# Kernel optimization log

Measured on AMD Instinct MI355X. Metric: run time of the kernel, lower is better.

## Reference

```python
import jax, jax.numpy as jnp
import numpy as np

B, C, L, D = 8, 16, 256, 512
DIM_HEAD = 64
SCALE = DIM_HEAD ** -0.5


def setup_inputs() -> dict:
    key = jax.random.key(0)
    ks = jax.random.split(key, 9)
    s = 0.05  # small init scale to keep activations sane
    return {
        "x": jax.random.normal(ks[0], (B, C, L, D), jnp.float32),
        "w_qkv": jax.random.normal(ks[1], (D, 3 * D), jnp.float32) * s,
        "pos_emb": jax.random.normal(ks[2], (1, C, L, L), jnp.float32),
        "w1": jax.random.normal(ks[3], (L, L), jnp.float32) * s,
        "b1": jnp.zeros((L,), jnp.float32),
        "w2": jax.random.normal(ks[4], (L, 1), jnp.float32) * s,
        "b2": jnp.zeros((1,), jnp.float32),
        "w_out": jax.random.normal(ks[5], (D, D), jnp.float32) * s,
        "b_out": jnp.zeros((D,), jnp.float32),
    }


def reference(x, w_qkv, pos_emb, w1, b1, w2, b2, w_out, b_out):
    # squared index distance |j - i|^2, shape [1,1,L,L]
    idx = jnp.arange(L, dtype=x.dtype)
    dist = ((idx[None, :] - idx[:, None]) ** 2)[None, None]

    qkv = jnp.einsum('bcld,de->bcle', x, w_qkv)  # [B,C,L,3D]
    q, k, v = jnp.split(qkv, 3, axis=-1)

    dots = jnp.einsum('bcld,bcmd->bclm', q, k) * SCALE  # [B,C,L,L]
    attn = jax.nn.softmax(dots, axis=-1)

    # per-row adaptive variance via small MLP over the score row
    attn_weight = attn + pos_emb                         # [B,C,L,L]
    h = jax.nn.relu(attn_weight @ w1 + b1)               # [B,C,L,L]
    w = h @ w2 + b2                                      # [B,C,L,1]

    # Gaussian distance decay, then second softmax
    weight = jnp.exp(-dist / (2.0 * w * w + 1e-6))       # [B,C,L,L]
    attn2 = jax.nn.softmax(attn * weight, axis=-1)

    out = jnp.einsum('bclm,bcmd->bcld', attn2, v)        # [B,C,L,D]
    return out @ w_out + b_out
```

## Files before the change

### kernel.cpp

```cpp
#include <hip/hip_runtime.h>
#include <hip/hip_bf16.h>

typedef unsigned short u16;
typedef unsigned int u32;

typedef short bf16x8 __attribute__((ext_vector_type(8)));
typedef float f32x4 __attribute__((ext_vector_type(4)));

__device__ __forceinline__ u16 f2bf(float f) {
    union { float f; u32 u; } v; v.f = f;
    u32 u = v.u;
    return (u16)((u + 0x7fffu + ((u >> 16) & 1u)) >> 16);
}
__device__ __forceinline__ float bf2f(u16 b) {
    union { u32 u; float f; } v; v.u = ((u32)b) << 16;
    return v.f;
}

__device__ __forceinline__ void gload16(const u16* g, u16* lds_uniform_base, int lane) {
#if __has_builtin(__builtin_amdgcn_global_load_lds)
    __builtin_amdgcn_global_load_lds((const __attribute__((address_space(1))) void*)g,
                                     (__attribute__((address_space(3))) void*)lds_uniform_base,
                                     16, 0, 0);
#else
    *(int4*)(lds_uniform_base + lane * 8) = *(const int4*)g;
#endif
}

#define MFMA_BF16 __builtin_amdgcn_mfma_f32_16x16x32_bf16

__global__ __launch_bounds__(256) void qkv_k(
    const u16* __restrict__ A, const u16* __restrict__ B, u16* __restrict__ C)
{
    __shared__ u16 As[2][4096];
    __shared__ u16 Bs[2][4096];
    const int tid  = threadIdx.x;
    const int lane = tid & 63;
    const int wave = tid >> 6;
    const int wm = (wave >> 1) * 64, wn = (wave & 1) * 64;
    const int row0 = blockIdx.x * 128;
    const int col0 = blockIdx.y * 128;
    const u16* Bb = B + (size_t)blockIdx.z * 262144;
    u16* Cb = C + (size_t)blockIdx.z * 16777216;
    const int l15 = lane & 15, l4 = lane >> 4;
    const int slotp = l4 ^ (lane & 3) ^ ((lane >> 2) & 3);

    f32x4 acc[4][4] = {};

    auto stage = [&](int buf, int k0) {
        #pragma unroll
        for (int i = 0; i < 2; ++i) {
            int idx = tid + i * 256;
            int r = idx >> 2, c = idx & 3;
            int s = c ^ (r & 3) ^ ((r >> 2) & 3);
            gload16(A + (size_t)(row0 + r) * 512 + k0 + s * 8, &As[buf][(idx & ~63) * 8], lane);
        }
        #pragma unroll
        for (int i = 0; i < 2; ++i) {
            int idx = tid + i * 256;
            int r = idx >> 2, c = idx & 3;
            int s = c ^ (r & 3) ^ ((r >> 2) & 3);
            gload16(Bb + (size_t)(col0 + r) * 512 + k0 + s * 8, &Bs[buf][(idx & ~63) * 8], lane);
        }
    };

    stage(0, 0);
    __syncthreads();
    for (int t = 0; t < 16; ++t) {
        int cur = t & 1;
        if (t < 15) stage(cur ^ 1, (t + 1) * 32);
        bf16x8 a[4], b[4];
        #pragma unroll
        for (int m = 0; m < 4; ++m)
            a[m] = *(const bf16x8*)&As[cur][(wm + m * 16 + l15) * 32 + slotp * 8];
        #pragma unroll
        for (int n = 0; n < 4; ++n)
            b[n] = *(const bf16x8*)&Bs[cur][(wn + n * 16 + l15) * 32 + slotp * 8];
        #pragma unroll
        for (int m = 0; m < 4; ++m)
            #pragma unroll
            for (int n = 0; n < 4; ++n)
                acc[m][n] = MFMA_BF16(a[m], b[n], acc[m][n], 0, 0, 0);
        __syncthreads();
    }

    #pragma unroll
    for (int m = 0; m < 4; ++m)
        #pragma unroll
        for (int n = 0; n < 4; ++n)
            #pragma unroll
            for (int r = 0; r < 4; ++r)
                Cb[(size_t)(row0 + wm + m * 16 + l4 * 4 + r) * 512 + col0 + wn + n * 16 + l15]
                    = f2bf(acc[m][n][r]);
}

__device__ __forceinline__ void stageB256(const u16* __restrict__ src, int ld, int k0,
                                          u16* buf, int tid, int lane) {
    #pragma unroll
    for (int i = 0; i < 4; ++i) {
        int idx = tid + i * 256;
        int r = idx >> 2, c = idx & 3;
        int s = c ^ (r & 3) ^ ((r >> 2) & 3);
        gload16(src + (size_t)r * ld + k0 + s * 8, &buf[(idx & ~63) * 8], lane);
    }
}
__device__ __forceinline__ void stageA64(const u16* __restrict__ src, int k0,
                                         u16* buf, int tid, int lane) {
    int r = tid >> 2, c = tid & 3;
    int s = c ^ (r & 3) ^ ((r >> 2) & 3);
    gload16(src + (size_t)r * 512 + k0 + s * 8, &buf[(tid & ~63) * 8], lane);
}

__device__ __forceinline__ int wswz(int row, int chunk) {
    return (chunk & 24) | ((chunk ^ row) & 7);
}
__device__ __forceinline__ bf16x8 rdW(const u16* W, int row, int chunk) {
    return *(const bf16x8*)&W[row * 256 + wswz(row, chunk) * 8];
}
__device__ __forceinline__ void wrW(u16* W, int row, int col, u16 v) {
    W[row * 256 + wswz(row, col >> 3) * 8 + (col & 7)] = v;
}

template<bool INIT>
__device__ __forceinline__ void gemm_from_W(
    f32x4 (&dst)[4][4], const u16* __restrict__ Bsrc, int ldb, int K,
    const u16* __restrict__ W, u16 (&Bs)[2][8192],
    int tid, int lane, int wn, int l15, int l4, int slotp)
{
    if (INIT)
        #pragma unroll
        for (int m = 0; m < 4; ++m)
            #pragma unroll
            for (int n = 0; n < 4; ++n) dst[m][n] = f32x4{0.f, 0.f, 0.f, 0.f};
    stageB256(Bsrc, ldb, 0, Bs[0], tid, lane);
    __syncthreads();
    const int nt = K >> 5;
    for (int t = 0; t < nt; ++t) {
        int cur = t & 1;
        if (t + 1 < nt) stageB256(Bsrc, ldb, (t + 1) * 32, Bs[cur ^ 1], tid, lane);
        bf16x8 a[4], b[4];
        #pragma unroll
        for (int m = 0; m < 4; ++m)
            a[m] = rdW(W, m * 16 + l15, t * 4 + l4);
        #pragma unroll
        for (int n = 0; n < 4; ++n)
            b[n] = *(const bf16x8*)&Bs[cur][(wn + n * 16 + l15) * 32 + slotp * 8];
        #pragma unroll
        for (int m = 0; m < 4; ++m)
            #pragma unroll
            for (int n = 0; n < 4; ++n)
                dst[m][n] = MFMA_BF16(a[m], b[n], dst[m][n], 0, 0, 0);
        __syncthreads();
    }
}

__device__ __forceinline__ void row_softmax(
    f32x4 (&val)[4][4], float (&red)[64][4], int wid, int l15, int l4)
{
    float rm[4][4];
    #pragma unroll
    for (int m = 0; m < 4; ++m)
        #pragma unroll
        for (int rr = 0; rr < 4; ++rr) {
            float x = fmaxf(fmaxf(val[m][0][rr], val[m][1][rr]),
                            fmaxf(val[m][2][rr], val[m][3][rr]));
            #pragma unroll
            for (int o = 1; o < 16; o <<= 1) x = fmaxf(x, __shfl_xor(x, o, 64));
            rm[m][rr] = x;
        }
    if (l15 == 0)
        #pragma unroll
        for (int m = 0; m < 4; ++m)
            #pragma unroll
            for (int rr = 0; rr < 4; ++rr)
                red[m * 16 + l4 * 4 + rr][wid] = rm[m][rr];
    __syncthreads();
    #pragma unroll
    for (int m = 0; m < 4; ++m)
        #pragma unroll
        for (int rr = 0; rr < 4; ++rr) {
            float4 rv = *(const float4*)&red[m * 16 + l4 * 4 + rr][0];
            rm[m][rr] = fmaxf(fmaxf(rv.x, rv.y), fmaxf(rv.z, rv.w));
        }
    __syncthreads();
    float rs[4][4];
    #pragma unroll
    for (int m = 0; m < 4; ++m)
        #pragma unroll
        for (int rr = 0; rr < 4; ++rr) {
            float s = 0.f;
            #pragma unroll
            for (int n = 0; n < 4; ++n) {
                float e = __expf(val[m][n][rr] - rm[m][rr]);
                val[m][n][rr] = e;
                s += e;
            }
            #pragma unroll
            for (int o = 1; o < 16; o <<= 1) s += __shfl_xor(s, o, 64);
            rs[m][rr] = s;
        }
    if (l15 == 0)
        #pragma unroll
        for (int m = 0; m < 4; ++m)
            #pragma unroll
            for (int rr = 0; rr < 4; ++rr)
                red[m * 16 + l4 * 4 + rr][wid] = rs[m][rr];
    __syncthreads();
    #pragma unroll
    for (int m = 0; m < 4; ++m)
        #pragma unroll
        for (int rr = 0; rr < 4; ++rr) {
            float4 rv = *(const float4*)&red[m * 16 + l4 * 4 + rr][0];
            float inv = 1.f / (rv.x + rv.y + rv.z + rv.w);
            #pragma unroll
            for (int n = 0; n < 4; ++n) val[m][n][rr] *= inv;
        }
    __syncthreads();
}

__global__ __launch_bounds__(256, 2) void fused_k(
    const u16* __restrict__ qb, const u16* __restrict__ kb, const u16* __restrict__ vT,
    const u16* __restrict__ w1T, const u16* __restrict__ woT,
    const float* __restrict__ pos, const float* __restrict__ b1v,
    const float* __restrict__ w2v, const float* __restrict__ b2v,
    const float* __restrict__ bov, float* __restrict__ out)
{
    __shared__ u16 As[2][2048];
    __shared__ u16 Bs[2][8192];
    __shared__ u16 W[64 * 256];
    __shared__ float red[64][4];
    __shared__ float wr[64];

    const int tid  = threadIdx.x;
    const int lane = tid & 63;
    const int wid  = tid >> 6;
    const int wn   = wid * 64;
    const int l15 = lane & 15, l4 = lane >> 4;
    const int slotp = l4 ^ (lane & 3) ^ ((lane >> 2) & 3);

    int hw = blockIdx.x + (blockIdx.y << 2);
    int wg = ((hw & 7) << 6) | (hw >> 3);
    const int row0 = (wg & 3) * 64;
    const int z    = wg >> 2;

    const u16* q = qb + (size_t)z * 131072 + (size_t)row0 * 512;
    const u16* k = kb + (size_t)z * 131072;
    const u16* v = vT + (size_t)z * 131072;
    const float* posb = pos + (size_t)(z & 15) * 65536 + (size_t)row0 * 256;
    const float b2s = b2v[0];

    f32x4 sa[4][4] = {};
    f32x4 acc[4][4];

    stageA64(q, 0, As[0], tid, lane);
    stageB256(k, 512, 0, Bs[0], tid, lane);
    __syncthreads();
    for (int t = 0; t < 16; ++t) {
        int cur = t & 1;
        if (t < 15) {
            stageA64(q, (t + 1) * 32, As[cur ^ 1], tid, lane);
            stageB256(k, 512, (t + 1) * 32, Bs[cur ^ 1], tid, lane);
        }
        bf16x8 a[4], b[4];
        #pragma unroll
        for (int m = 0; m < 4; ++m)
            a[m] = *(const bf16x8*)&As[cur][(m * 16 + l15) * 32 + slotp * 8];
        #pragma unroll
        for (int n = 0; n < 4; ++n)
            b[n] = *(const bf16x8*)&Bs[cur][(wn + n * 16 + l15) * 32 + slotp * 8];
        #pragma unroll
        for (int m = 0; m < 4; ++m)
            #pragma unroll
            for (int n = 0; n < 4; ++n)
                sa[m][n] = MFMA_BF16(a[m], b[n], sa[m][n], 0, 0, 0);
        __syncthreads();
    }

    #pragma unroll
    for (int m = 0; m < 4; ++m)
        #pragma unroll
        for (int n = 0; n < 4; ++n) sa[m][n] *= 0.125f;
    row_softmax(sa, red, wid, l15, l4);
    #pragma unroll
    for (int m = 0; m < 4; ++m)
        #pragma unroll
        for (int rr = 0; rr < 4; ++rr) {
            int row = m * 16 + l4 * 4 + rr;
            #pragma unroll
            for (int n = 0; n < 4; ++n) {
                int col = wn + n * 16 + l15;
                wrW(W, row, col, f2bf(sa[m][n][rr] + posb[row * 256 + col]));
            }
        }

    float b1c[4], w2c[4];
    #pragma unroll
    for (int n = 0; n < 4; ++n) {
        int col = wn + n * 16 + l15;
        b1c[n] = b1v[col];
        w2c[n] = w2v[col];
    }
    gemm_from_W<true>(acc, w1T, 256, 256, W, Bs, tid, lane, wn, l15, l4, slotp);
    {
        float part[4][4];
        #pragma unroll
        for (int m = 0; m < 4; ++m)
            #pragma unroll
            for (int rr = 0; rr < 4; ++rr) {
                float p = 0.f;
                #pragma unroll
                for (int n = 0; n < 4; ++n)
                    p += fmaxf(acc[m][n][rr] + b1c[n], 0.f) * w2c[n];
                #pragma unroll
                for (int o = 1; o < 16; o <<= 1) p += __shfl_xor(p, o, 64);
                part[m][rr] = p;
            }
        if (l15 == 0)
            #pragma unroll
            for (int m = 0; m < 4; ++m)
                #pragma unroll
                for (int rr = 0; rr < 4; ++rr)
                    red[m * 16 + l4 * 4 + rr][wid] = part[m][rr];
        __syncthreads();
        if (wid == 0 && l15 == 0)
            #pragma unroll
            for (int m = 0; m < 4; ++m)
                #pragma unroll
                for (int rr = 0; rr < 4; ++rr) {
                    int row = m * 16 + l4 * 4 + rr;
                    float4 rv = *(const float4*)&red[row][0];
                    wr[row] = rv.x + rv.y + rv.z + rv.w + b2s;
                }
        __syncthreads();
    }

    #pragma unroll
    for (int m = 0; m < 4; ++m)
        #pragma unroll
        for (int rr = 0; rr < 4; ++rr) {
            int row = m * 16 + l4 * 4 + rr;
            float wv = wr[row];
            float idn = 1.f / (2.f * wv * wv + 1e-6f);
            int rg = row0 + row;
            #pragma unroll
            for (int n = 0; n < 4; ++n) {
                float d = (float)(wn + n * 16 + l15 - rg);
                sa[m][n][rr] *= __expf(-d * d * idn);
            }
        }
    row_softmax(sa, red, wid, l15, l4);
    #pragma unroll
    for (int m = 0; m < 4; ++m)
        #pragma unroll
        for (int rr = 0; rr < 4; ++rr) {
            int row = m * 16 + l4 * 4 + rr;
            #pragma unroll
            for (int n = 0; n < 4; ++n)
                wrW(W, row, wn + n * 16 + l15, f2bf(sa[m][n][rr]));
        }
    __syncthreads();

    gemm_from_W<true>(sa,  v,         256, 256, W, Bs, tid, lane, wn, l15, l4, slotp);
    gemm_from_W<true>(acc, v + 65536, 256, 256, W, Bs, tid, lane, wn, l15, l4, slotp);

    #pragma unroll
    for (int m = 0; m < 4; ++m)
        #pragma unroll
        for (int rr = 0; rr < 4; ++rr) {
            int row = m * 16 + l4 * 4 + rr;
            #pragma unroll
            for (int n = 0; n < 4; ++n)
                wrW(W, row, wn + n * 16 + l15, f2bf(sa[m][n][rr]));
        }
    f32x4 o0[4][4], o1[4][4];
    gemm_from_W<true>(o0, woT,                512, 256, W, Bs, tid, lane, wn, l15, l4, slotp);
    gemm_from_W<true>(o1, woT + 131072,       512, 256, W, Bs, tid, lane, wn, l15, l4, slotp);
    #pragma unroll
    for (int m = 0; m < 4; ++m)
        #pragma unroll
        for (int rr = 0; rr < 4; ++rr) {
            int row = m * 16 + l4 * 4 + rr;
            #pragma unroll
            for (int n = 0; n < 4; ++n)
                wrW(W, row, wn + n * 16 + l15, f2bf(acc[m][n][rr]));
        }
    gemm_from_W<false>(o0, woT + 256,          512, 256, W, Bs, tid, lane, wn, l15, l4, slotp);
    gemm_from_W<false>(o1, woT + 131072 + 256, 512, 256, W, Bs, tid, lane, wn, l15, l4, slotp);

    float bo0[4], bo1[4];
    #pragma unroll
    for (int n = 0; n < 4; ++n) {
        bo0[n] = bov[wn + n * 16 + l15];
        bo1[n] = bov[256 + wn + n * 16 + l15];
    }
    #pragma unroll
    for (int m = 0; m < 4; ++m)
        #pragma unroll
        for (int rr = 0; rr < 4; ++rr) {
            int row = row0 + m * 16 + l4 * 4 + rr;
            size_t ob = ((size_t)z * 256 + row) * 512;
            #pragma unroll
            for (int n = 0; n < 4; ++n) {
                out[ob + wn + n * 16 + l15]       = o0[m][n][rr] + bo0[n];
                out[ob + 256 + wn + n * 16 + l15] = o1[m][n][rr] + bo1[n];
            }
        }
}

__global__ __launch_bounds__(256) void trans_f2b_k(
    const float* __restrict__ in, u16* __restrict__ out, int R, int C)
{
    __shared__ u16 t[64][80];
    const int bx = blockIdx.x, by = blockIdx.y;
    const int tid = threadIdx.x;
    const int r = tid >> 2, c16 = (tid & 3) * 16;
    const float* ip = in + (size_t)(by * 64 + r) * C + bx * 64 + c16;
    #pragma unroll
    for (int j = 0; j < 4; ++j) {
        float4 vv = *(const float4*)(ip + j * 4);
        t[r][c16 + j * 4 + 0] = f2bf(vv.x);
        t[r][c16 + j * 4 + 1] = f2bf(vv.y);
        t[r][c16 + j * 4 + 2] = f2bf(vv.z);
        t[r][c16 + j * 4 + 3] = f2bf(vv.w);
    }
    __syncthreads();
    const int orow = tid >> 2, oc = (tid & 3) * 16;
    u16 o[16];
    #pragma unroll
    for (int j = 0; j < 16; ++j) o[j] = t[oc + j][orow];
    u16* op = out + (size_t)(bx * 64 + orow) * R + by * 64 + oc;
    *(int4*)op       = *(const int4*)&o[0];
    *(int4*)(op + 8) = *(const int4*)&o[8];
}

__global__ __launch_bounds__(256) void trans_b2b_k(
    const u16* __restrict__ in, u16* __restrict__ out,
    int ldin, int R, long sIn, long sOut)
{
    __shared__ u16 t[64][80];
    const int bx = blockIdx.x, by = blockIdx.y;
    const long zz = blockIdx.z;
    const u16* ip = in + zz * sIn;
    u16* op = out + zz * sOut;
    const int tid = threadIdx.x;
    const int r = tid >> 2, c16 = (tid & 3) * 16;
    const u16* src = ip + (size_t)(by * 64 + r) * ldin + bx * 64 + c16;
    *(int4*)&t[r][c16]     = *(const int4*)src;
    *(int4*)&t[r][c16 + 8] = *(const int4*)(src + 8);
    __syncthreads();
    const int orow = tid >> 2, oc = (tid & 3) * 16;
    u16 o[16];
    #pragma unroll
    for (int j = 0; j < 16; ++j) o[j] = t[oc + j][orow];
    u16* dst = op + (size_t)(bx * 64 + orow) * R + by * 64 + oc;
    *(int4*)dst       = *(const int4*)&o[0];
    *(int4*)(dst + 8) = *(const int4*)&o[8];
}

__global__ __launch_bounds__(256) void conv_b_k(
    const float* __restrict__ in, u16* __restrict__ out, int n8)
{
    int i = blockIdx.x * 256 + threadIdx.x;
    if (i >= n8) return;
    float4 a = ((const float4*)in)[i * 2], b = ((const float4*)in)[i * 2 + 1];
    u16 o[8] = { f2bf(a.x), f2bf(a.y), f2bf(a.z), f2bf(a.w),
                 f2bf(b.x), f2bf(b.y), f2bf(b.z), f2bf(b.w) };
    ((int4*)out)[i] = *(const int4*)o;
}

extern "C" void kernel_launch(void* const* d_in, const int* in_sizes, int n_in,
                              void* d_out, int out_size, void* d_ws, size_t ws_size,
                              hipStream_t stream) {
    const float* x     = (const float*)d_in[0];
    const float* w_qkv = (const float*)d_in[1];
    const float* pos   = (const float*)d_in[2];
    const float* w1    = (const float*)d_in[3];
    const float* b1    = (const float*)d_in[4];
    const float* w2    = (const float*)d_in[5];
    const float* b2    = (const float*)d_in[6];
    const float* w_out = (const float*)d_in[7];
    const float* b_out = (const float*)d_in[8];
    float* out = (float*)d_out;
    char* ws = (char*)d_ws;

    u16* xb    = (u16*)(ws);
    u16* vT    = (u16*)(ws);
    u16* qkvb  = (u16*)(ws + 33554432);
    u16* wqkvT = (u16*)(ws + 134217728);
    u16* w1T   = (u16*)(ws + 135790592);
    u16* woT   = (u16*)(ws + 135921664);
    if (ws_size < (size_t)136445952) return;

    u16* qb = qkvb;
    u16* kb = qkvb + 16777216;
    u16* vb = qkvb + 33554432;

    dim3 blk(256);

    conv_b_k<<<dim3(8192), blk, 0, stream>>>(x, xb, 2097152);
    trans_f2b_k<<<dim3(24, 8), blk, 0, stream>>>(w_qkv, wqkvT, 512, 1536);
    trans_f2b_k<<<dim3(4, 4), blk, 0, stream>>>(w1, w1T, 256, 256);
    trans_f2b_k<<<dim3(8, 8), blk, 0, stream>>>(w_out, woT, 512, 512);

    qkv_k<<<dim3(256, 4, 3), blk, 0, stream>>>(xb, wqkvT, qkvb);

    trans_b2b_k<<<dim3(8, 4, 128), blk, 0, stream>>>(vb, vT, 512, 256, 131072L, 131072L);

    fused_k<<<dim3(4, 128), blk, 0, stream>>>(
        qb, kb, vT, w1T, woT, pos, b1, w2, b2, b_out, out);
}
```

Baseline: 334.7 us.

## Replace LDS-staged operand tiles with direct global fragment loads in GEMMs

Removes the double-buffered LDS staging and global_load_lds paths for B operands (and Q/K and the QKV GEMM) so each wave reads MFMA fragments directly from global memory via L1/L2, dropping per-iteration barriers. The fused kernel now keeps two LDS attention/value tiles (Wa, Wb) and restructures the output projection into a loop over halves with fewer live accumulators. qkv_k gets a higher occupancy hint. This trades LDS traffic and syncs for uncoalesced-ish redundant global/cache loads across waves and less latency hiding.

```diff
diff --git a/kernel.cpp b/kernel.cpp
--- a/kernel.cpp
+++ b/kernel.cpp
@@ -17,23 +17,11 @@
     return v.f;
 }
 
-__device__ __forceinline__ void gload16(const u16* g, u16* lds_uniform_base, int lane) {
-#if __has_builtin(__builtin_amdgcn_global_load_lds)
-    __builtin_amdgcn_global_load_lds((const __attribute__((address_space(1))) void*)g,
-                                     (__attribute__((address_space(3))) void*)lds_uniform_base,
-                                     16, 0, 0);
-#else
-    *(int4*)(lds_uniform_base + lane * 8) = *(const int4*)g;
-#endif
-}
-
 #define MFMA_BF16 __builtin_amdgcn_mfma_f32_16x16x32_bf16
 
-__global__ __launch_bounds__(256) void qkv_k(
+__global__ __launch_bounds__(256, 3) void qkv_k(
     const u16* __restrict__ A, const u16* __restrict__ B, u16* __restrict__ C)
 {
-    __shared__ u16 As[2][4096];
-    __shared__ u16 Bs[2][4096];
     const int tid  = threadIdx.x;
     const int lane = tid & 63;
     const int wave = tid >> 6;
@@ -43,45 +31,26 @@
     const u16* Bb = B + (size_t)blockIdx.z * 262144;
     u16* Cb = C + (size_t)blockIdx.z * 16777216;
     const int l15 = lane & 15, l4 = lane >> 4;
-    const int slotp = l4 ^ (lane & 3) ^ ((lane >> 2) & 3);
+
+    const u16* Arow = A + (size_t)(row0 + wm + l15) * 512 + l4 * 8;
+    const u16* Brow = Bb + (size_t)(col0 + wn + l15) * 512 + l4 * 8;
 
     f32x4 acc[4][4] = {};
 
-    auto stage = [&](int buf, int k0) {
-        #pragma unroll
-        for (int i = 0; i < 2; ++i) {
-            int idx = tid + i * 256;
-            int r = idx >> 2, c = idx & 3;
-            int s = c ^ (r & 3) ^ ((r >> 2) & 3);
-            gload16(A + (size_t)(row0 + r) * 512 + k0 + s * 8, &As[buf][(idx & ~63) * 8], lane);
-        }
-        #pragma unroll
-        for (int i = 0; i < 2; ++i) {
-            int idx = tid + i * 256;
-            int r = idx >> 2, c = idx & 3;
-            int s = c ^ (r & 3) ^ ((r >> 2) & 3);
-            gload16(Bb + (size_t)(col0 + r) * 512 + k0 + s * 8, &Bs[buf][(idx & ~63) * 8], lane);
-        }
-    };
-
-    stage(0, 0);
-    __syncthreads();
+    #pragma unroll 4
     for (int t = 0; t < 16; ++t) {
-        int cur = t & 1;
-        if (t < 15) stage(cur ^ 1, (t + 1) * 32);
         bf16x8 a[4], b[4];
         #pragma unroll
         for (int m = 0; m < 4; ++m)
-            a[m] = *(const bf16x8*)&As[cur][(wm + m * 16 + l15) * 32 + slotp * 8];
+            a[m] = *(const bf16x8*)(Arow + (size_t)m * 16 * 512 + t * 32);
         #pragma unroll
         for (int n = 0; n < 4; ++n)
-            b[n] = *(const bf16x8*)&Bs[cur][(wn + n * 16 + l15) * 32 + slotp * 8];
+            b[n] = *(const bf16x8*)(Brow + (size_t)n * 16 * 512 + t * 32);
         #pragma unroll
         for (int m = 0; m < 4; ++m)
             #pragma unroll
             for (int n = 0; n < 4; ++n)
                 acc[m][n] = MFMA_BF16(a[m], b[n], acc[m][n], 0, 0, 0);
-        __syncthreads();
     }
 
     #pragma unroll
@@ -94,23 +63,6 @@
                     = f2bf(acc[m][n][r]);
 }
 
-__device__ __forceinline__ void stageB256(const u16* __restrict__ src, int ld, int k0,
-                                          u16* buf, int tid, int lane) {
-    #pragma unroll
-    for (int i = 0; i < 4; ++i) {
-        int idx = tid + i * 256;
-        int r = idx >> 2, c = idx & 3;
-        int s = c ^ (r & 3) ^ ((r >> 2) & 3);
-        gload16(src + (size_t)r * ld + k0 + s * 8, &buf[(idx & ~63) * 8], lane);
-    }
-}
-__device__ __forceinline__ void stageA64(const u16* __restrict__ src, int k0,
-                                         u16* buf, int tid, int lane) {
-    int r = tid >> 2, c = tid & 3;
-    int s = c ^ (r & 3) ^ ((r >> 2) & 3);
-    gload16(src + (size_t)r * 512 + k0 + s * 8, &buf[(tid & ~63) * 8], lane);
-}
-
 __device__ __forceinline__ int wswz(int row, int chunk) {
     return (chunk & 24) | ((chunk ^ row) & 7);
 }
@@ -122,35 +74,30 @@
 }
 
 template<bool INIT>
-__device__ __forceinline__ void gemm_from_W(
-    f32x4 (&dst)[4][4], const u16* __restrict__ Bsrc, int ldb, int K,
-    const u16* __restrict__ W, u16 (&Bs)[2][8192],
-    int tid, int lane, int wn, int l15, int l4, int slotp)
-{
-    if (INIT)
+__device__ __forceinline__ void gemm_WB(
+    f32x4 (&dst)[4][4], const u16* __restrict__ Wlds, const u16* __restrict__ Bg,
+    int ldb, int wn, int l15, int l4)
+{
+    if constexpr (INIT)
         #pragma unroll
         for (int m = 0; m < 4; ++m)
             #pragma unroll
             for (int n = 0; n < 4; ++n) dst[m][n] = f32x4{0.f, 0.f, 0.f, 0.f};
-    stageB256(Bsrc, ldb, 0, Bs[0], tid, lane);
-    __syncthreads();
-    const int nt = K >> 5;
-    for (int t = 0; t < nt; ++t) {
-        int cur = t & 1;
-        if (t + 1 < nt) stageB256(Bsrc, ldb, (t + 1) * 32, Bs[cur ^ 1], tid, lane);
+    const u16* Brow = Bg + (size_t)(wn + l15) * ldb + l4 * 8;
+    #pragma unroll 4
+    for (int t = 0; t < 8; ++t) {
         bf16x8 a[4], b[4];
         #pragma unroll
         for (int m = 0; m < 4; ++m)
-            a[m] = rdW(W, m * 16 + l15, t * 4 + l4);
+            a[m] = rdW(Wlds, m * 16 + l15, t * 4 + l4);
         #pragma unroll
         for (int n = 0; n < 4; ++n)
-            b[n] = *(const bf16x8*)&Bs[cur][(wn + n * 16 + l15) * 32 + slotp * 8];
+            b[n] = *(const bf16x8*)(Brow + (size_t)n * 16 * ldb + t * 32);
         #pragma unroll
         for (int m = 0; m < 4; ++m)
             #pragma unroll
             for (int n = 0; n < 4; ++n)
                 dst[m][n] = MFMA_BF16(a[m], b[n], dst[m][n], 0, 0, 0);
-        __syncthreads();
     }
 }
 
@@ -225,9 +172,8 @@
     const float* __restrict__ w2v, const float* __restrict__ b2v,
     const float* __restrict__ bov, float* __restrict__ out)
 {
-    __shared__ u16 As[2][2048];
-    __shared__ u16 Bs[2][8192];
-    __shared__ u16 W[64 * 256];
+    __shared__ u16 Wa[64 * 256];
+    __shared__ u16 Wb[64 * 256];
     __shared__ float red[64][4];
     __shared__ float wr[64];
 
@@ -236,7 +182,6 @@
     const int wid  = tid >> 6;
     const int wn   = wid * 64;
     const int l15 = lane & 15, l4 = lane >> 4;
-    const int slotp = l4 ^ (lane & 3) ^ ((lane >> 2) & 3);
 
     int hw = blockIdx.x + (blockIdx.y << 2);
     int wg = ((hw & 7) << 6) | (hw >> 3);
@@ -252,28 +197,24 @@
     f32x4 sa[4][4] = {};
     f32x4 acc[4][4];
 
-    stageA64(q, 0, As[0], tid, lane);
-    stageB256(k, 512, 0, Bs[0], tid, lane);
-    __syncthreads();
-    for (int t = 0; t < 16; ++t) {
-        int cur = t & 1;
-        if (t < 15) {
-            stageA64(q, (t + 1) * 32, As[cur ^ 1], tid, lane);
-            stageB256(k, 512, (t + 1) * 32, Bs[cur ^ 1], tid, lane);
-        }
-        bf16x8 a[4], b[4];
-        #pragma unroll
-        for (int m = 0; m < 4; ++m)
-            a[m] = *(const bf16x8*)&As[cur][(m * 16 + l15) * 32 + slotp * 8];
-        #pragma unroll
-        for (int n = 0; n < 4; ++n)
-            b[n] = *(const bf16x8*)&Bs[cur][(wn + n * 16 + l15) * 32 + slotp * 8];
-        #pragma unroll
-        for (int m = 0; m < 4; ++m)
-            #pragma unroll
-            for (int n = 0; n < 4; ++n)
-                sa[m][n] = MFMA_BF16(a[m], b[n], sa[m][n], 0, 0, 0);
-        __syncthreads();
+    {
+        const u16* qrow = q + (size_t)l15 * 512 + l4 * 8;
+        const u16* krow = k + (size_t)(wn + l15) * 512 + l4 * 8;
+        #pragma unroll 4
+        for (int t = 0; t < 16; ++t) {
+            bf16x8 a[4], b[4];
+            #pragma unroll
+            for (int m = 0; m < 4; ++m)
+                a[m] = *(const bf16x8*)(qrow + (size_t)m * 16 * 512 + t * 32);
+            #pragma unroll
+            for (int n = 0; n < 4; ++n)
+                b[n] = *(const bf16x8*)(krow + (size_t)n * 16 * 512 + t * 32);
+            #pragma unroll
+            for (int m = 0; m < 4; ++m)
+                #pragma unroll
+                for (int n = 0; n < 4; ++n)
+                    sa[m][n] = MFMA_BF16(a[m], b[n], sa[m][n], 0, 0, 0);
+        }
     }
 
     #pragma unroll
@@ -289,9 +230,10 @@
             #pragma unroll
             for (int n = 0; n < 4; ++n) {
                 int col = wn + n * 16 + l15;
-                wrW(W, row, col, f2bf(sa[m][n][rr] + posb[row * 256 + col]));
+                wrW(Wa, row, col, f2bf(sa[m][n][rr] + posb[row * 256 + col]));
             }
         }
+    __syncthreads();
 
     float b1c[4], w2c[4];
     #pragma unroll
@@ -300,7 +242,7 @@
         b1c[n] = b1v[col];
         w2c[n] = w2v[col];
     }
-    gemm_from_W<true>(acc, w1T, 256, 256, W, Bs, tid, lane, wn, l15, l4, slotp);
+    gemm_WB<true>(acc, Wa, w1T, 256, wn, l15, l4);
     {
         float part[4][4];
         #pragma unroll
@@ -356,13 +298,11 @@
             int row = m * 16 + l4 * 4 + rr;
             #pragma unroll
             for (int n = 0; n < 4; ++n)
-                wrW(W, row, wn + n * 16 + l15, f2bf(sa[m][n][rr]));
-        }
-    __syncthreads();
-
-    gemm_from_W<true>(sa,  v,         256, 256, W, Bs, tid, lane, wn, l15, l4, slotp);
-    gemm_from_W<true>(acc, v + 65536, 256, 256, W, Bs, tid, lane, wn, l15, l4, slotp);
-
+                wrW(Wa, row, wn + n * 16 + l15, f2bf(sa[m][n][rr]));
+        }
+    __syncthreads();
+
+    gemm_WB<true>(acc, Wa, v, 256, wn, l15, l4);
     #pragma unroll
     for (int m = 0; m < 4; ++m)
         #pragma unroll
@@ -370,11 +310,10 @@
             int row = m * 16 + l4 * 4 + rr;
             #pragma unroll
             for (int n = 0; n < 4; ++n)
-                wrW(W, row, wn + n * 16 + l15, f2bf(sa[m][n][rr]));
-        }
-    f32x4 o0[4][4], o1[4][4];
-    gemm_from_W<true>(o0, woT,                512, 256, W, Bs, tid, lane, wn, l15, l4, slotp);
-    gemm_from_W<true>(o1, woT + 131072,       512, 256, W, Bs, tid, lane, wn, l15, l4, slotp);
+                wrW(Wb, row, wn + n * 16 + l15, f2bf(acc[m][n][rr]));
+        }
+    gemm_WB<true>(acc, Wa, v + 65536, 256, wn, l15, l4);
+    __syncthreads();
     #pragma unroll
     for (int m = 0; m < 4; ++m)
         #pragma unroll
@@ -382,29 +321,28 @@
             int row = m * 16 + l4 * 4 + rr;
             #pragma unroll
             for (int n = 0; n < 4; ++n)
-                wrW(W, row, wn + n * 16 + l15, f2bf(acc[m][n][rr]));
-        }
-    gemm_from_W<false>(o0, woT + 256,          512, 256, W, Bs, tid, lane, wn, l15, l4, slotp);
-    gemm_from_W<false>(o1, woT + 131072 + 256, 512, 256, W, Bs, tid, lane, wn, l15, l4, slotp);
-
-    float bo0[4], bo1[4];
-    #pragma unroll
-    for (int n = 0; n < 4; ++n) {
-        bo0[n] = bov[wn + n * 16 + l15];
-        bo1[n] = bov[256 + wn + n * 16 + l15];
-    }
-    #pragma unroll
-    for (int m = 0; m < 4; ++m)
-        #pragma unroll
-        for (int rr = 0; rr < 4; ++rr) {
-            int row = row0 + m * 16 + l4 * 4 + rr;
-            size_t ob = ((size_t)z * 256 + row) * 512;
-            #pragma unroll
-            for (int n = 0; n < 4; ++n) {
-                out[ob + wn + n * 16 + l15]       = o0[m][n][rr] + bo0[n];
-                out[ob + 256 + wn + n * 16 + l15] = o1[m][n][rr] + bo1[n];
+                wrW(Wa, row, wn + n * 16 + l15, f2bf(acc[m][n][rr]));
+        }
+    __syncthreads();
+
+    for (int nh = 0; nh < 2; ++nh) {
+        f32x4 o[4][4];
+        gemm_WB<true >(o, Wb, woT + (size_t)nh * 131072,       512, wn, l15, l4);
+        gemm_WB<false>(o, Wa, woT + (size_t)nh * 131072 + 256, 512, wn, l15, l4);
+        float boc[4];
+        #pragma unroll
+        for (int n = 0; n < 4; ++n) boc[n] = bov[nh * 256 + wn + n * 16 + l15];
+        #pragma unroll
+        for (int m = 0; m < 4; ++m)
+            #pragma unroll
+            for (int rr = 0; rr < 4; ++rr) {
+                int row = row0 + m * 16 + l4 * 4 + rr;
+                size_t ob = ((size_t)z * 256 + row) * 512 + nh * 256;
+                #pragma unroll
+                for (int n = 0; n < 4; ++n)
+                    out[ob + wn + n * 16 + l15] = o[m][n][rr] + boc[n];
             }
-        }
+    }
 }
 
 __global__ __launch_bounds__(256) void trans_f2b_k(
```

After: 440.1 us. 1.31x slower.
